# Kernel optimization log

Hardware: AMD Instinct MI355X
Metric: run time of the kernel (lower is better)

The kernel has to match this reference:

```python
import jax, jax.numpy as jnp
import numpy as np

D_MODEL, N_HEADS, D_K, D_V = 1024, 16, 64, 64
B, S = 4, 1024
LN_EPS = 1e-5


def setup_inputs() -> dict:
    key = jax.random.key(0)
    ks = jax.random.split(key, 12)
    s = 0.02
    # causal mask: True = masked (mimics masked_fill_ semantics)
    mask = jnp.triu(jnp.ones((S, S), dtype=bool), k=1)
    mask = jnp.broadcast_to(mask, (B, S, S))
    return {
        "Q": jax.random.normal(ks[0], (B, S, D_MODEL), jnp.float32),
        "K": jax.random.normal(ks[1], (B, S, D_MODEL), jnp.float32),
        "V": jax.random.normal(ks[2], (B, S, D_MODEL), jnp.float32),
        "mask": mask,
        # Linear params stored as [in, out] (equivalent to torch weight.T)
        "Wq": jax.random.normal(ks[3], (D_MODEL, N_HEADS * D_K), jnp.float32) * s,
        "bq": jnp.zeros((N_HEADS * D_K,), jnp.float32),
        "Wk": jax.random.normal(ks[4], (D_MODEL, N_HEADS * D_K), jnp.float32) * s,
        "bk": jnp.zeros((N_HEADS * D_K,), jnp.float32),
        "Wv": jax.random.normal(ks[5], (D_MODEL, N_HEADS * D_V), jnp.float32) * s,
        "bv": jnp.zeros((N_HEADS * D_V,), jnp.float32),
        "Wo": jax.random.normal(ks[6], (N_HEADS * D_V, D_MODEL), jnp.float32) * s,
        "bo": jnp.zeros((D_MODEL,), jnp.float32),
        "gamma": jnp.ones((D_MODEL,), jnp.float32),
        "beta": jnp.zeros((D_MODEL,), jnp.float32),
    }


def reference(Q, K, V, mask, Wq, bq, Wk, bk, Wv, bv, Wo, bo, gamma, beta):
    b, sq, _ = Q.shape
    sk = K.shape[1]
    residual = Q
    # projections -> [b, h, s, d]
    q = (Q @ Wq + bq).reshape(b, sq, N_HEADS, D_K).transpose(0, 2, 1, 3)
    k = (K @ Wk + bk).reshape(b, sk, N_HEADS, D_K).transpose(0, 2, 1, 3)
    v = (V @ Wv + bv).reshape(b, sk, N_HEADS, D_V).transpose(0, 2, 1, 3)
    scale = 1.0 / np.sqrt(D_K).astype(np.float32)
    scores = jnp.einsum("bhqd,bhkd->bhqk", q, k) * scale  # [b,h,sq,sk]
    scores = jnp.where(mask[:, None, :, :], jnp.float32(-1e9), scores)
    attn = jax.nn.softmax(scores, axis=-1)
    out = jnp.einsum("bhqk,bhkd->bhqd", attn, v)
    out = out.transpose(0, 2, 1, 3).reshape(b, sq, N_HEADS * D_V)
    out = out @ Wo + bo
    # LayerNorm(out + residual)
    x = out + residual
    mu = jnp.mean(x, axis=-1, keepdims=True)
    var = jnp.mean(jnp.square(x - mu), axis=-1, keepdims=True)
    y = (x - mu) * jax.lax.rsqrt(var + LN_EPS) * gamma + beta
    return (y, attn)
```

## Files before the change

### kernel.cpp

```cpp
#include <hip/hip_runtime.h>
#include <stdint.h>

#define B_ 4
#define S_ 1024
#define H_ 16
#define D_ 64
#define DM 1024
#define M_ (B_*S_)

typedef unsigned short ushort_t;
typedef unsigned int u32;
using bf16x8 = __attribute__((ext_vector_type(8))) short;
using f32x4  = __attribute__((ext_vector_type(4))) float;

__device__ inline ushort_t f2bf(float f) {
  unsigned u = __float_as_uint(f);
  u += 0x7fff + ((u >> 16) & 1);
  return (ushort_t)(u >> 16);
}
__device__ inline float bf2f(ushort_t s) {
  return __uint_as_float(((unsigned)s) << 16);
}

__device__ __forceinline__ void gl2lds16(const void* g, void* l) {
  __builtin_amdgcn_global_load_lds(
      (const __attribute__((address_space(1))) u32*)g,
      (__attribute__((address_space(3))) u32*)l,
      16, 0, 0);
}

__global__ __launch_bounds__(256) void cvt_f32_bf16(const float* __restrict__ src,
                                                    ushort_t* __restrict__ dst, int n4) {
  int i = blockIdx.x * 256 + threadIdx.x;
  if (i < n4) {
    float4 v = ((const float4*)src)[i];
    ushort4 o;
    o.x = f2bf(v.x); o.y = f2bf(v.y); o.z = f2bf(v.z); o.w = f2bf(v.w);
    ((ushort4*)dst)[i] = o;
  }
}

__global__ __launch_bounds__(256) void transpose_cvt(const float* w0, const float* w1,
                                                     const float* w2, const float* w3,
                                                     ushort_t* o0, ushort_t* o1,
                                                     ushort_t* o2, ushort_t* o3) {
  const float* src; ushort_t* dst;
  switch (blockIdx.z) {
    case 0: src = w0; dst = o0; break;
    case 1: src = w1; dst = o1; break;
    case 2: src = w2; dst = o2; break;
    default: src = w3; dst = o3; break;
  }
  float scl = (blockIdx.z == 0) ? 0.125f : 1.0f;
  __shared__ float t[32][33];
  int tx = threadIdx.x, ty = threadIdx.y;
  int x = blockIdx.x * 32 + tx;
  for (int i = 0; i < 4; i++) {
    int y = blockIdx.y * 32 + ty + i * 8;
    t[ty + i * 8][tx] = src[y * DM + x];
  }
  __syncthreads();
  int xo = blockIdx.y * 32 + tx;
  for (int i = 0; i < 4; i++) {
    int yo = blockIdx.x * 32 + ty + i * 8;
    dst[yo * DM + xo] = f2bf(t[tx][ty + i * 8] * scl);
  }
}

#define BM 64
#define BN 128
__global__ __launch_bounds__(256, 4) void gemm_nt(const ushort_t* __restrict__ X,
                                                  const ushort_t* __restrict__ WT,
                                                  const float* __restrict__ bias, float bscale,
                                                  void* __restrict__ out, int mode) {
  __shared__ ushort_t Al[BM][32];
  __shared__ ushort_t Bl[BN][32];
  int t = threadIdx.x;
  int lane = t & 63, w = t >> 6, quad = lane >> 4, l16 = lane & 15;
  int wm = w & 1, wn = w >> 1;
  int m0 = blockIdx.y * BM, n0 = blockIdx.x * BN;
  f32x4 acc[2][4] = {};
  int r4 = t >> 2, c8 = (t & 3) * 8;
  const ushort_t* ga  = X  + (size_t)(m0 + r4) * DM + c8;
  const ushort_t* gb0 = WT + (size_t)(n0 + r4) * DM + c8;
  const ushort_t* gb1 = WT + (size_t)(n0 + 64 + r4) * DM + c8;
  ushort_t* la  = &Al[r4][c8];
  ushort_t* lb0 = &Bl[r4][c8];
  ushort_t* lb1 = &Bl[64 + r4][c8];
  for (int k0 = 0; k0 < DM; k0 += 32) {
    gl2lds16(ga  + k0, la);
    gl2lds16(gb0 + k0, lb0);
    gl2lds16(gb1 + k0, lb1);
    __syncthreads();
    bf16x8 af[2], bfv[4];
    for (int ms = 0; ms < 2; ms++) af[ms]  = *(const bf16x8*)&Al[wm * 32 + ms * 16 + l16][quad * 8];
    for (int ns = 0; ns < 4; ns++) bfv[ns] = *(const bf16x8*)&Bl[wn * 64 + ns * 16 + l16][quad * 8];
    for (int ms = 0; ms < 2; ms++)
      for (int ns = 0; ns < 4; ns++)
        acc[ms][ns] = __builtin_amdgcn_mfma_f32_16x16x32_bf16(af[ms], bfv[ns], acc[ms][ns], 0, 0, 0);
    __syncthreads();
  }
  for (int ms = 0; ms < 2; ms++)
    for (int ns = 0; ns < 4; ns++)
      for (int r = 0; r < 4; r++) {
        int gm = m0 + wm * 32 + ms * 16 + quad * 4 + r;
        int gn = n0 + wn * 64 + ns * 16 + l16;
        float v = acc[ms][ns][r] + bias[gn] * bscale;
        if (mode == 2) {
          ((float*)out)[(size_t)gm * DM + gn] = v;
        } else {
          int b = gm >> 10, s = gm & 1023, h = gn >> 6, d = gn & 63;
          if (mode == 0)
            ((ushort_t*)out)[(((size_t)(b * H_ + h)) * S_ + s) * D_ + d] = f2bf(v);
          else
            ((ushort_t*)out)[(((size_t)(b * H_ + h)) * D_ + d) * S_ + s] = f2bf(v);
        }
      }
}

__global__ __launch_bounds__(256) void attn_kernel(const ushort_t* __restrict__ qp,
                                                   const ushort_t* __restrict__ kp,
                                                   const ushort_t* __restrict__ vT,
                                                   float* __restrict__ attn_out,
                                                   ushort_t* __restrict__ ctx) {
  __shared__ ushort_t Srow[16][1032];
  __shared__ float red[16][16];
  __shared__ float rmax[16];
  __shared__ float rinv[16];
  int t = threadIdx.x;
  int lane = t & 63, w = t >> 6, quad = lane >> 4, l16 = lane & 15;
  int bx = blockIdx.x;
  int qt = bx & 63, h = (bx >> 6) & 15, b = bx >> 10;
  int bh = b * H_ + h;
  const int L = (qt + 1) * 16;

  const ushort_t* qbase = qp + (((size_t)bh * S_) + qt * 16 + l16) * D_;
  for (int ct = w; ct <= qt; ct += 4) {
    f32x4 acc = {};
    for (int d0 = 0; d0 < 64; d0 += 32) {
      bf16x8 af  = *(const bf16x8*)&qbase[d0 + quad * 8];
      bf16x8 bfr = *(const bf16x8*)&kp[(((size_t)bh * S_) + ct * 16 + l16) * D_ + d0 + quad * 8];
      acc = __builtin_amdgcn_mfma_f32_16x16x32_bf16(af, bfr, acc, 0, 0, 0);
    }
    for (int r = 0; r < 4; r++) {
      int row = quad * 4 + r;
      int gq = qt * 16 + row, gk = ct * 16 + l16;
      Srow[row][ct * 16 + l16] = f2bf((gk <= gq) ? acc[r] : -1e30f);
    }
  }
  __syncthreads();

  int row = t >> 4, sub = t & 15;
  float m = -1e30f;
  for (int i = 0; i < 8; i++) {
    int c = (sub + 16 * i) * 8;
    if (c < L) {
      bf16x8 v = *(const bf16x8*)&Srow[row][c];
      for (int j = 0; j < 8; j++) m = fmaxf(m, bf2f((ushort_t)v[j]));
    }
  }
  red[row][sub] = m;
  __syncthreads();
  if (t < 16) {
    float mm = -1e30f;
    for (int j = 0; j < 16; j++) mm = fmaxf(mm, red[t][j]);
    rmax[t] = mm;
  }
  __syncthreads();

  float mr = rmax[row], sum = 0.f;
  for (int i = 0; i < 8; i++) {
    int c = (sub + 16 * i) * 8;
    if (c < L) {
      bf16x8 v = *(const bf16x8*)&Srow[row][c];
      bf16x8 e;
      for (int j = 0; j < 8; j++) {
        float ev = __expf(bf2f((ushort_t)v[j]) - mr);
        e[j] = (short)f2bf(ev);
        sum += ev;
      }
      *(bf16x8*)&Srow[row][c] = e;
    }
  }
  red[row][sub] = sum;
  __syncthreads();
  if (t < 16) {
    float l = 0.f;
    for (int j = 0; j < 16; j++) l += red[t][j];
    rinv[t] = 1.0f / l;
  }
  __syncthreads();

  float* outbase = attn_out + (((size_t)bh) * S_ + qt * 16) * S_;
  float ri = rinv[row];
  for (int i = 0; i < 8; i++) {
    int c = (sub + 16 * i) * 8;
    float4 o0 = {0.f, 0.f, 0.f, 0.f}, o1 = {0.f, 0.f, 0.f, 0.f};
    if (c < L) {
      bf16x8 v = *(const bf16x8*)&Srow[row][c];
      o0.x = bf2f((ushort_t)v[0]) * ri; o0.y = bf2f((ushort_t)v[1]) * ri;
      o0.z = bf2f((ushort_t)v[2]) * ri; o0.w = bf2f((ushort_t)v[3]) * ri;
      o1.x = bf2f((ushort_t)v[4]) * ri; o1.y = bf2f((ushort_t)v[5]) * ri;
      o1.z = bf2f((ushort_t)v[6]) * ri; o1.w = bf2f((ushort_t)v[7]) * ri;
    }
    *(float4*)&outbase[(size_t)row * S_ + c]     = o0;
    *(float4*)&outbase[(size_t)row * S_ + c + 4] = o1;
  }
  if (L & 31) {
    Srow[t & 15][L + (t >> 4)] = 0;
  }
  __syncthreads();

  int K32 = (L + 31) >> 5;
  f32x4 oacc = {};
  int n = w * 16 + l16;
  for (int kk = 0; kk < K32; kk++) {
    int k0 = kk * 32;
    bf16x8 af  = *(const bf16x8*)&Srow[l16][k0 + quad * 8];
    bf16x8 bfr = *(const bf16x8*)&vT[(((size_t)bh) * D_ + n) * S_ + k0 + quad * 8];
    oacc = __builtin_amdgcn_mfma_f32_16x16x32_bf16(af, bfr, oacc, 0, 0, 0);
  }
  for (int r = 0; r < 4; r++) {
    int rr = quad * 4 + r;
    ctx[(((size_t)b * S_) + qt * 16 + rr) * DM + h * D_ + n] = f2bf(oacc[r] * rinv[rr]);
  }
}

__global__ __launch_bounds__(256) void ln_kernel(const float* __restrict__ y0,
                                                 const float* __restrict__ resid,
                                                 const float* __restrict__ gamma,
                                                 const float* __restrict__ beta,
                                                 float* __restrict__ out) {
  int row = blockIdx.x, t = threadIdx.x;
  float x[4]; float s = 0.f, s2 = 0.f;
  for (int i = 0; i < 4; i++) {
    int c = t + i * 256;
    float v = y0[(size_t)row * DM + c] + resid[(size_t)row * DM + c];
    x[i] = v; s += v; s2 += v * v;
  }
  for (int off = 32; off; off >>= 1) {
    s  += __shfl_down(s,  off, 64);
    s2 += __shfl_down(s2, off, 64);
  }
  __shared__ float ws1[4], ws2[4];
  __shared__ float mu_s, rv_s;
  int wv = t >> 6, lane = t & 63;
  if (lane == 0) { ws1[wv] = s; ws2[wv] = s2; }
  __syncthreads();
  if (t == 0) {
    float ts = ws1[0] + ws1[1] + ws1[2] + ws1[3];
    float ts2 = ws2[0] + ws2[1] + ws2[2] + ws2[3];
    float mu = ts / DM;
    float var = ts2 / DM - mu * mu;
    mu_s = mu; rv_s = rsqrtf(var + 1e-5f);
  }
  __syncthreads();
  float mu = mu_s, rv = rv_s;
  for (int i = 0; i < 4; i++) {
    int c = t + i * 256;
    out[(size_t)row * DM + c] = (x[i] - mu) * rv * gamma[c] + beta[c];
  }
}

extern "C" void kernel_launch(void* const* d_in, const int* in_sizes, int n_in,
                              void* d_out, int out_size, void* d_ws, size_t ws_size,
                              hipStream_t stream) {
  const float* Qf = (const float*)d_in[0];
  const float* Kf = (const float*)d_in[1];
  const float* Vf = (const float*)d_in[2];
  const float* Wq = (const float*)d_in[4];
  const float* bq = (const float*)d_in[5];
  const float* Wk = (const float*)d_in[6];
  const float* bk = (const float*)d_in[7];
  const float* Wv = (const float*)d_in[8];
  const float* bv = (const float*)d_in[9];
  const float* Wo = (const float*)d_in[10];
  const float* bo = (const float*)d_in[11];
  const float* gamma = (const float*)d_in[12];
  const float* beta  = (const float*)d_in[13];

  char* ws = (char*)d_ws;
  unsigned short* Qb  = (unsigned short*)(ws + 0);
  unsigned short* ctx = (unsigned short*)(ws + 0);
  unsigned short* Kb  = (unsigned short*)(ws + 8388608);
  unsigned short* Vb  = (unsigned short*)(ws + 16777216);
  float*          y0  = (float*)(ws + 8388608);
  unsigned short* WqT = (unsigned short*)(ws + 25165824);
  unsigned short* WkT = (unsigned short*)(ws + 27262976);
  unsigned short* WvT = (unsigned short*)(ws + 29360128);
  unsigned short* WoT = (unsigned short*)(ws + 31457280);
  unsigned short* qp  = (unsigned short*)(ws + 33554432);
  unsigned short* kp  = (unsigned short*)(ws + 41943040);
  unsigned short* vTp = (unsigned short*)(ws + 50331648);

  float* y_out    = (float*)d_out;
  float* attn_out = (float*)d_out + (size_t)M_ * DM;

  int n4 = M_ * DM / 4;
  cvt_f32_bf16<<<dim3(n4 / 256), dim3(256), 0, stream>>>(Qf, Qb, n4);
  cvt_f32_bf16<<<dim3(n4 / 256), dim3(256), 0, stream>>>(Kf, Kb, n4);
  cvt_f32_bf16<<<dim3(n4 / 256), dim3(256), 0, stream>>>(Vf, Vb, n4);
  transpose_cvt<<<dim3(32, 32, 4), dim3(32, 8), 0, stream>>>(Wq, Wk, Wv, Wo, WqT, WkT, WvT, WoT);

  dim3 ggrid(DM / BN, M_ / BM);
  gemm_nt<<<ggrid, 256, 0, stream>>>(Qb, WqT, bq, 0.125f, qp, 0);
  gemm_nt<<<ggrid, 256, 0, stream>>>(Kb, WkT, bk, 1.0f, kp, 0);
  gemm_nt<<<ggrid, 256, 0, stream>>>(Vb, WvT, bv, 1.0f, vTp, 1);

  attn_kernel<<<dim3(B_ * H_ * (S_ / 16)), 256, 0, stream>>>(qp, kp, vTp, attn_out, ctx);

  gemm_nt<<<ggrid, 256, 0, stream>>>(ctx, WoT, bo, 1.0f, y0, 2);
  ln_kernel<<<dim3(M_), 256, 0, stream>>>(y0, Qf, gamma, beta, y_out);
}
```

Measured before the change: 542.5 us.

## Batch QKV projections, widen GEMM tiles, and use 32-row attention tiles

Merges the three input conversion kernels into one launch and the three QKV projection GEMMs into a single grid-z launch. Widens the GEMM tile from 64x128 to 64x256 with 4x4 MFMA accumulators per wave, lowering the occupancy hint. Doubles the attention query tile to 32 rows with 512 threads, so Q fragments and K loads are reused across two 16-row halves. The trade-off is fewer blocks, more registers and more LDS per block, which may hurt occupancy and load balance on the causal triangle.

```diff
diff --git a/kernel.cpp b/kernel.cpp
--- a/kernel.cpp
+++ b/kernel.cpp
@@ -29,15 +29,23 @@
       16, 0, 0);
 }
 
-__global__ __launch_bounds__(256) void cvt_f32_bf16(const float* __restrict__ src,
-                                                    ushort_t* __restrict__ dst, int n4) {
+__global__ __launch_bounds__(256) void cvt3(const float* __restrict__ q,
+                                            const float* __restrict__ k,
+                                            const float* __restrict__ v,
+                                            ushort_t* __restrict__ qo,
+                                            ushort_t* __restrict__ ko,
+                                            ushort_t* __restrict__ vo) {
+  const float* src; ushort_t* dst;
+  switch (blockIdx.y) {
+    case 0: src = q; dst = qo; break;
+    case 1: src = k; dst = ko; break;
+    default: src = v; dst = vo; break;
+  }
   int i = blockIdx.x * 256 + threadIdx.x;
-  if (i < n4) {
-    float4 v = ((const float4*)src)[i];
-    ushort4 o;
-    o.x = f2bf(v.x); o.y = f2bf(v.y); o.z = f2bf(v.z); o.w = f2bf(v.w);
-    ((ushort4*)dst)[i] = o;
-  }
+  float4 val = ((const float4*)src)[i];
+  ushort4 o;
+  o.x = f2bf(val.x); o.y = f2bf(val.y); o.z = f2bf(val.z); o.w = f2bf(val.w);
+  ((ushort4*)dst)[i] = o;
 }
 
 __global__ __launch_bounds__(256) void transpose_cvt(const float* w0, const float* w1,
@@ -67,44 +75,48 @@
   }
 }
 
-#define BM 64
-#define BN 128
-__global__ __launch_bounds__(256, 4) void gemm_nt(const ushort_t* __restrict__ X,
-                                                  const ushort_t* __restrict__ WT,
-                                                  const float* __restrict__ bias, float bscale,
-                                                  void* __restrict__ out, int mode) {
-  __shared__ ushort_t Al[BM][32];
-  __shared__ ushort_t Bl[BN][32];
+__device__ __forceinline__ void gemm_core(const ushort_t* __restrict__ X,
+                                          const ushort_t* __restrict__ WT,
+                                          const float* __restrict__ bias, float bscale,
+                                          void* __restrict__ out, int mode,
+                                          int bx, int by) {
+  __shared__ ushort_t Al[64][32];
+  __shared__ ushort_t Bl[256][32];
   int t = threadIdx.x;
   int lane = t & 63, w = t >> 6, quad = lane >> 4, l16 = lane & 15;
-  int wm = w & 1, wn = w >> 1;
-  int m0 = blockIdx.y * BM, n0 = blockIdx.x * BN;
-  f32x4 acc[2][4] = {};
+  int m0 = by * 64, n0 = bx * 256;
+  f32x4 acc[4][4] = {};
   int r4 = t >> 2, c8 = (t & 3) * 8;
-  const ushort_t* ga  = X  + (size_t)(m0 + r4) * DM + c8;
-  const ushort_t* gb0 = WT + (size_t)(n0 + r4) * DM + c8;
-  const ushort_t* gb1 = WT + (size_t)(n0 + 64 + r4) * DM + c8;
+  const ushort_t* ga = X + (size_t)(m0 + r4) * DM + c8;
+  const ushort_t* gb0 = WT + (size_t)(n0 +   0 + r4) * DM + c8;
+  const ushort_t* gb1 = WT + (size_t)(n0 +  64 + r4) * DM + c8;
+  const ushort_t* gb2 = WT + (size_t)(n0 + 128 + r4) * DM + c8;
+  const ushort_t* gb3 = WT + (size_t)(n0 + 192 + r4) * DM + c8;
   ushort_t* la  = &Al[r4][c8];
   ushort_t* lb0 = &Bl[r4][c8];
   ushort_t* lb1 = &Bl[64 + r4][c8];
+  ushort_t* lb2 = &Bl[128 + r4][c8];
+  ushort_t* lb3 = &Bl[192 + r4][c8];
   for (int k0 = 0; k0 < DM; k0 += 32) {
-    gl2lds16(ga  + k0, la);
+    gl2lds16(ga + k0, la);
     gl2lds16(gb0 + k0, lb0);
     gl2lds16(gb1 + k0, lb1);
+    gl2lds16(gb2 + k0, lb2);
+    gl2lds16(gb3 + k0, lb3);
     __syncthreads();
-    bf16x8 af[2], bfv[4];
-    for (int ms = 0; ms < 2; ms++) af[ms]  = *(const bf16x8*)&Al[wm * 32 + ms * 16 + l16][quad * 8];
-    for (int ns = 0; ns < 4; ns++) bfv[ns] = *(const bf16x8*)&Bl[wn * 64 + ns * 16 + l16][quad * 8];
-    for (int ms = 0; ms < 2; ms++)
+    bf16x8 af[4], bfv[4];
+    for (int ms = 0; ms < 4; ms++) af[ms]  = *(const bf16x8*)&Al[ms * 16 + l16][quad * 8];
+    for (int ns = 0; ns < 4; ns++) bfv[ns] = *(const bf16x8*)&Bl[w * 64 + ns * 16 + l16][quad * 8];
+    for (int ms = 0; ms < 4; ms++)
       for (int ns = 0; ns < 4; ns++)
         acc[ms][ns] = __builtin_amdgcn_mfma_f32_16x16x32_bf16(af[ms], bfv[ns], acc[ms][ns], 0, 0, 0);
     __syncthreads();
   }
-  for (int ms = 0; ms < 2; ms++)
+  for (int ms = 0; ms < 4; ms++)
     for (int ns = 0; ns < 4; ns++)
       for (int r = 0; r < 4; r++) {
-        int gm = m0 + wm * 32 + ms * 16 + quad * 4 + r;
-        int gn = n0 + wn * 64 + ns * 16 + l16;
+        int gm = m0 + ms * 16 + quad * 4 + r;
+        int gn = n0 + w * 64 + ns * 16 + l16;
         float v = acc[ms][ns][r] + bias[gn] * bscale;
         if (mode == 2) {
           ((float*)out)[(size_t)gm * DM + gn] = v;
@@ -118,34 +130,62 @@
       }
 }
 
-__global__ __launch_bounds__(256) void attn_kernel(const ushort_t* __restrict__ qp,
+__global__ __launch_bounds__(256, 2) void gemm_qkv(const ushort_t* Qb, const ushort_t* Kb,
+                                                   const ushort_t* Vb,
+                                                   const ushort_t* WqT, const ushort_t* WkT,
+                                                   const ushort_t* WvT,
+                                                   const float* bq, const float* bk,
+                                                   const float* bv,
+                                                   ushort_t* qp, ushort_t* kp, ushort_t* vTp) {
+  int z = blockIdx.z;
+  const ushort_t* X  = (z == 0) ? Qb  : (z == 1) ? Kb  : Vb;
+  const ushort_t* WT = (z == 0) ? WqT : (z == 1) ? WkT : WvT;
+  const float* bias  = (z == 0) ? bq  : (z == 1) ? bk  : bv;
+  ushort_t* out      = (z == 0) ? qp  : (z == 1) ? kp  : vTp;
+  float bscale = (z == 0) ? 0.125f : 1.0f;
+  int mode = (z == 2) ? 1 : 0;
+  gemm_core(X, WT, bias, bscale, out, mode, blockIdx.x, blockIdx.y);
+}
+
+__global__ __launch_bounds__(256, 2) void gemm_o(const ushort_t* ctx, const ushort_t* WoT,
+                                                 const float* bo, float* y0) {
+  gemm_core(ctx, WoT, bo, 1.0f, y0, 2, blockIdx.x, blockIdx.y);
+}
+
+__global__ __launch_bounds__(512) void attn_kernel(const ushort_t* __restrict__ qp,
                                                    const ushort_t* __restrict__ kp,
                                                    const ushort_t* __restrict__ vT,
                                                    float* __restrict__ attn_out,
                                                    ushort_t* __restrict__ ctx) {
-  __shared__ ushort_t Srow[16][1032];
-  __shared__ float red[16][16];
-  __shared__ float rmax[16];
-  __shared__ float rinv[16];
+  __shared__ ushort_t Srow[32][1048];
+  __shared__ float red[32][16];
+  __shared__ float rmax[32];
+  __shared__ float rinv[32];
   int t = threadIdx.x;
   int lane = t & 63, w = t >> 6, quad = lane >> 4, l16 = lane & 15;
   int bx = blockIdx.x;
-  int qt = bx & 63, h = (bx >> 6) & 15, b = bx >> 10;
+  int qt = bx & 31, h = (bx >> 5) & 15, b = bx >> 9;
   int bh = b * H_ + h;
-  const int L = (qt + 1) * 16;
-
-  const ushort_t* qbase = qp + (((size_t)bh * S_) + qt * 16 + l16) * D_;
-  for (int ct = w; ct <= qt; ct += 4) {
-    f32x4 acc = {};
-    for (int d0 = 0; d0 < 64; d0 += 32) {
-      bf16x8 af  = *(const bf16x8*)&qbase[d0 + quad * 8];
-      bf16x8 bfr = *(const bf16x8*)&kp[(((size_t)bh * S_) + ct * 16 + l16) * D_ + d0 + quad * 8];
-      acc = __builtin_amdgcn_mfma_f32_16x16x32_bf16(af, bfr, acc, 0, 0, 0);
-    }
-    for (int r = 0; r < 4; r++) {
-      int row = quad * 4 + r;
-      int gq = qt * 16 + row, gk = ct * 16 + l16;
-      Srow[row][ct * 16 + l16] = f2bf((gk <= gq) ? acc[r] : -1e30f);
+  const int L = (qt + 1) * 32;
+  const int nct = (qt + 1) * 2;
+
+  bf16x8 af[2][2];
+  for (int mh = 0; mh < 2; mh++)
+    for (int dh = 0; dh < 2; dh++)
+      af[mh][dh] = *(const bf16x8*)&qp[(((size_t)bh * S_) + qt * 32 + mh * 16 + l16) * D_ + dh * 32 + quad * 8];
+
+  for (int ct = w; ct < nct; ct += 8) {
+    bf16x8 bk0 = *(const bf16x8*)&kp[(((size_t)bh * S_) + ct * 16 + l16) * D_ + 0  + quad * 8];
+    bf16x8 bk1 = *(const bf16x8*)&kp[(((size_t)bh * S_) + ct * 16 + l16) * D_ + 32 + quad * 8];
+    for (int mh = 0; mh < 2; mh++) {
+      f32x4 acc = {};
+      acc = __builtin_amdgcn_mfma_f32_16x16x32_bf16(af[mh][0], bk0, acc, 0, 0, 0);
+      acc = __builtin_amdgcn_mfma_f32_16x16x32_bf16(af[mh][1], bk1, acc, 0, 0, 0);
+      for (int r = 0; r < 4; r++) {
+        int row = mh * 16 + quad * 4 + r;
+        int gq = qt * 32 + row, gk = ct * 16 + l16;
+        Srow[row][ct * 16 + l16] = f2bf((gk <= gq) ? acc[r] : -1e30f);
+      }
     }
   }
   __syncthreads();
@@ -161,7 +201,7 @@
   }
   red[row][sub] = m;
   __syncthreads();
-  if (t < 16) {
+  if (t < 32) {
     float mm = -1e30f;
     for (int j = 0; j < 16; j++) mm = fmaxf(mm, red[t][j]);
     rmax[t] = mm;
@@ -184,14 +224,14 @@
   }
   red[row][sub] = sum;
   __syncthreads();
-  if (t < 16) {
+  if (t < 32) {
     float l = 0.f;
     for (int j = 0; j < 16; j++) l += red[t][j];
     rinv[t] = 1.0f / l;
   }
   __syncthreads();
 
-  float* outbase = attn_out + (((size_t)bh) * S_ + qt * 16) * S_;
+  float* outbase = attn_out + (((size_t)bh) * S_ + qt * 32) * S_;
   float ri = rinv[row];
   for (int i = 0; i < 8; i++) {
     int c = (sub + 16 * i) * 8;
@@ -206,23 +246,20 @@
     *(float4*)&outbase[(size_t)row * S_ + c]     = o0;
     *(float4*)&outbase[(size_t)row * S_ + c + 4] = o1;
   }
-  if (L & 31) {
-    Srow[t & 15][L + (t >> 4)] = 0;
-  }
-  __syncthreads();
-
-  int K32 = (L + 31) >> 5;
+  __syncthreads();
+
+  int mh = w & 1;
+  int n = (w >> 1) * 16 + l16;
   f32x4 oacc = {};
-  int n = w * 16 + l16;
-  for (int kk = 0; kk < K32; kk++) {
+  for (int kk = 0; kk <= qt; kk++) {
     int k0 = kk * 32;
-    bf16x8 af  = *(const bf16x8*)&Srow[l16][k0 + quad * 8];
+    bf16x8 ea  = *(const bf16x8*)&Srow[mh * 16 + l16][k0 + quad * 8];
     bf16x8 bfr = *(const bf16x8*)&vT[(((size_t)bh) * D_ + n) * S_ + k0 + quad * 8];
-    oacc = __builtin_amdgcn_mfma_f32_16x16x32_bf16(af, bfr, oacc, 0, 0, 0);
+    oacc = __builtin_amdgcn_mfma_f32_16x16x32_bf16(ea, bfr, oacc, 0, 0, 0);
   }
   for (int r = 0; r < 4; r++) {
-    int rr = quad * 4 + r;
-    ctx[(((size_t)b * S_) + qt * 16 + rr) * DM + h * D_ + n] = f2bf(oacc[r] * rinv[rr]);
+    int rr = mh * 16 + quad * 4 + r;
+    ctx[(((size_t)b * S_) + qt * 32 + rr) * DM + h * D_ + n] = f2bf(oacc[r] * rinv[rr]);
   }
 }
 
@@ -297,18 +334,14 @@
   float* attn_out = (float*)d_out + (size_t)M_ * DM;
 
   int n4 = M_ * DM / 4;
-  cvt_f32_bf16<<<dim3(n4 / 256), dim3(256), 0, stream>>>(Qf, Qb, n4);
-  cvt_f32_bf16<<<dim3(n4 / 256), dim3(256), 0, stream>>>(Kf, Kb, n4);
-  cvt_f32_bf16<<<dim3(n4 / 256), dim3(256), 0, stream>>>(Vf, Vb, n4);
+  cvt3<<<dim3(n4 / 256, 3), 256, 0, stream>>>(Qf, Kf, Vf, Qb, Kb, Vb);
   transpose_cvt<<<dim3(32, 32, 4), dim3(32, 8), 0, stream>>>(Wq, Wk, Wv, Wo, WqT, WkT, WvT, WoT);
 
-  dim3 ggrid(DM / BN, M_ / BM);
-  gemm_nt<<<ggrid, 256, 0, stream>>>(Qb, WqT, bq, 0.125f, qp, 0);
-  gemm_nt<<<ggrid, 256, 0, stream>>>(Kb, WkT, bk, 1.0f, kp, 0);
-  gemm_nt<<<ggrid, 256, 0, stream>>>(Vb, WvT, bv, 1.0f, vTp, 1);
-
-  attn_kernel<<<dim3(B_ * H_ * (S_ / 16)), 256, 0, stream>>>(qp, kp, vTp, attn_out, ctx);
-
-  gemm_nt<<<ggrid, 256, 0, stream>>>(ctx, WoT, bo, 1.0f, y0, 2);
+  gemm_qkv<<<dim3(DM / 256, M_ / 64, 3), 256, 0, stream>>>(Qb, Kb, Vb, WqT, WkT, WvT,
+                                                           bq, bk, bv, qp, kp, vTp);
+
+  attn_kernel<<<dim3(B_ * H_ * (S_ / 32)), 512, 0, stream>>>(qp, kp, vTp, attn_out, ctx);
+
+  gemm_o<<<dim3(DM / 256, M_ / 64), 256, 0, stream>>>(ctx, WoT, bo, y0);
   ln_kernel<<<dim3(M_), 256, 0, stream>>>(y0, Qf, gamma, beta, y_out);
 }
```

Measured after the change: 534.2 us. No clear change (-1.5%).
